# Optimization experiments

Measured on AMD Instinct MI355X. Metric: run time of the kernel, lower is better.

## Reference

```python
import jax, jax.numpy as jnp
import numpy as np

B = 32768
EPS = 0.2  # BatchNorm eps used in the original module


def _xavier(key, shape):
    fan_in, fan_out = shape[-2], shape[-1]
    std = (2.0 / (fan_in + fan_out)) ** 0.5
    return (jax.random.normal(key, shape, jnp.float32) * std).astype(jnp.float32)


def bn(x, g, b):
    # training-mode BatchNorm1d: batch stats over the batch axis (-2), biased var
    m = jnp.mean(x, axis=-2, keepdims=True)
    v = jnp.mean(jnp.square(x - m), axis=-2, keepdims=True)
    return (x - m) * jax.lax.rsqrt(v + EPS) * g + b


def setup_inputs() -> dict:
    key = jax.random.key(0)
    ks = iter(jax.random.split(key, 48))
    inp = {}
    inp['x1f'] = jax.random.normal(next(ks), (B, 512), jnp.float32)
    inp['x2f'] = jax.random.normal(next(ks), (B, 512), jnp.float32)
    # shared trunk
    inp['W1'] = _xavier(next(ks), (512, 256)); inp['b1'] = jnp.zeros(256, jnp.float32)
    inp['W2'] = _xavier(next(ks), (256, 256)); inp['b2'] = jnp.zeros(256, jnp.float32)
    # batchnorm affine params (bn1:256, bn2:256, bn3:128, bn4:64)
    inp['g1'] = jnp.ones(256, jnp.float32); inp['be1'] = jnp.zeros(256, jnp.float32)
    inp['g2'] = jnp.ones(256, jnp.float32); inp['be2'] = jnp.zeros(256, jnp.float32)
    inp['g3'] = jnp.ones(128, jnp.float32); inp['be3'] = jnp.zeros(128, jnp.float32)
    inp['g4'] = jnp.ones(64, jnp.float32); inp['be4'] = jnp.zeros(64, jnp.float32)
    # 4 branch projections from each stream (x11..x14, x21..x24), stacked on axis 0
    inp['Wbx1'] = _xavier(next(ks), (4, 256, 256)); inp['bbx1'] = jnp.zeros((4, 256), jnp.float32)
    inp['Wbx2'] = _xavier(next(ks), (4, 256, 256)); inp['bbx2'] = jnp.zeros((4, 256), jnp.float32)
    # gating MLPs (xw*1, xw*2, xw*3, y*), stacked over the 4 attributes
    inp['Wwa'] = _xavier(next(ks), (4, 512, 128)); inp['bwa'] = jnp.zeros((4, 128), jnp.float32)
    inp['Wwb'] = _xavier(next(ks), (4, 128, 64)); inp['bwb'] = jnp.zeros((4, 64), jnp.float32)
    inp['Wwc'] = _xavier(next(ks), (4, 64, 64)); inp['bwc'] = jnp.zeros((4, 64), jnp.float32)
    inp['Wy'] = _xavier(next(ks), (4, 64, 2)); inp['by'] = jnp.zeros((4, 2), jnp.float32)
    # combine layers x1c..x4c, stacked
    inp['Wc'] = _xavier(next(ks), (4, 512, 256)); inp['bc'] = jnp.zeros((4, 256), jnp.float32)
    # output heads (different class counts: 3, 3, 6, 4)
    inp['Wo1'] = _xavier(next(ks), (256, 3)); inp['bo1'] = jnp.zeros(3, jnp.float32)
    inp['Wo2'] = _xavier(next(ks), (256, 3)); inp['bo2'] = jnp.zeros(3, jnp.float32)
    inp['Wo3'] = _xavier(next(ks), (256, 6)); inp['bo3'] = jnp.zeros(6, jnp.float32)
    inp['Wo4'] = _xavier(next(ks), (256, 4)); inp['bo4'] = jnp.zeros(4, jnp.float32)
    return inp


def reference(x1f, x2f, W1, b1, W2, b2, g1, be1, g2, be2, g3, be3, g4, be4,
              Wbx1, bbx1, Wbx2, bbx2, Wwa, bwa, Wwb, bwb, Wwc, bwc, Wy, by,
              Wc, bc, Wo1, bo1, Wo2, bo2, Wo3, bo3, Wo4, bo4):
    relu = jax.nn.relu

    def trunk(x):
        h = bn(relu(x @ W1 + b1), g1, be1)
        return bn(relu(h @ W2 + b2), g2, be2)

    h1 = trunk(x1f)  # [B,256]
    h2 = trunk(x2f)  # [B,256]

    # 4 branch features per stream, each bn1-normalized: [4,B,256]
    b1x = bn(relu(jnp.einsum('bi,kio->kbo', h1, Wbx1) + bbx1[:, None, :]), g1, be1)
    b2x = bn(relu(jnp.einsum('bi,kio->kbo', h2, Wbx2) + bbx2[:, None, :]), g1, be1)

    # gating MLP per attribute -> 2-way softmax weights
    xcat = jnp.concatenate([b1x, b2x], axis=-1)  # [4,B,512]
    a = bn(relu(jnp.einsum('kbi,kio->kbo', xcat, Wwa) + bwa[:, None, :]), g3, be3)
    b_ = bn(relu(jnp.einsum('kbi,kio->kbo', a, Wwb) + bwb[:, None, :]), g4, be4)
    c = bn(relu(jnp.einsum('kbi,kio->kbo', b_, Wwc) + bwc[:, None, :]), g4, be4)
    y = jax.nn.softmax(jnp.einsum('kbi,kio->kbo', c, Wy) + by[:, None, :], axis=-1)  # [4,B,2]

    # the original per-column loop == one broadcast multiply per stream
    xw = jnp.concatenate([b1x * y[..., 0:1], b2x * y[..., 1:2]], axis=-1)  # [4,B,512]

    # combine layers (dropout is identity in eval)
    xc = bn(relu(jnp.einsum('kbi,kio->kbo', xw, Wc) + bc[:, None, :]), g1, be1)  # [4,B,256]

    y1o = jax.nn.softmax(xc[0] @ Wo1 + bo1, axis=-1)
    y2o = jax.nn.softmax(xc[1] @ Wo2 + bo2, axis=-1)
    y3o = jax.nn.softmax(xc[2] @ Wo3 + bo3, axis=-1)
    y4o = jax.nn.softmax(xc[3] @ Wo4 + bo4, axis=-1)
    return (y1o, y2o, y3o, y4o)
```

## Files before the change

### kernel.cpp

```cpp
#include <hip/hip_runtime.h>
#include <hip/hip_bf16.h>


typedef unsigned short u16;
typedef _Float16 f16x8 __attribute__((ext_vector_type(8)));
typedef float f32x4 __attribute__((ext_vector_type(4)));

#define B_ROWS 32768
#define EPS_BN 0.2f
#define BINV (1.0f / 32768.0f)

__device__ __forceinline__ float bf2f(u16 u) {
    union { unsigned int i; float f; } c;
    c.i = ((unsigned int)u) << 16;
    return c.f;
}
__device__ __forceinline__ u16 f2bf(float f) {
    union { float f; unsigned int i; } c;
    c.f = f;
    unsigned int x = c.i;
    return (u16)((x + 0x7FFFu + ((x >> 16) & 1u)) >> 16);
}
__device__ __forceinline__ float h2f(u16 u) {
    _Float16 h;
    __builtin_memcpy(&h, &u, 2);
    return (float)h;
}
__device__ __forceinline__ u16 f2h(float f) {
    _Float16 h = (_Float16)f;
    u16 u;
    __builtin_memcpy(&u, &h, 2);
    return u;
}
__device__ __forceinline__ float ldp(const void* p, long i, int flag) {
    return flag ? bf2f(((const u16*)p)[i]) : ((const float*)p)[i];
}
__device__ __forceinline__ void gload16(const u16* gp, u16* lp) {
    __builtin_amdgcn_global_load_lds(
        (const __attribute__((address_space(1))) unsigned int*)gp,
        (__attribute__((address_space(3))) unsigned int*)lp, 16, 0, 0);
}

__global__ void detect_dtype(const u16* __restrict__ x, int* __restrict__ flag) {
    const int lane = threadIdx.x;
    const u16 v = x[2 * lane];
    const int e = (v >> 7) & 0xFF;
    const bool plausible = (e >= 110 && e <= 140);
    const unsigned long long m = __ballot(plausible);
    if (lane == 0) *flag = (__popcll(m) >= 58) ? 1 : 0;
}

struct PTab { const void* p[20]; int n[20]; int off[20]; };

__global__ void convert_params(PTab t, float* __restrict__ dst,
                               const int* __restrict__ flag) {
    const int ti = blockIdx.y;
    const int n = t.n[ti];
    float* o = dst + t.off[ti];
    const int isbf = *flag;
    for (int i = blockIdx.x * 256 + threadIdx.x; i < n; i += gridDim.x * 256)
        o[i] = ldp(t.p[ti], i, isbf);
}

__global__ __launch_bounds__(256) void prep_w(
    const void* __restrict__ W, long wstride,
    const void* __restrict__ bias, long bstride,
    const float* __restrict__ psum, const float* __restrict__ psq, int pstride,
    const void* __restrict__ pg, const void* __restrict__ pbe, int gmask,
    const int* __restrict__ dtflag,
    u16* __restrict__ Wt, long wtstride,
    float* __restrict__ biasP, float* __restrict__ T0o,
    float* __restrict__ T1o, float* __restrict__ bsum, long bost,
    int K, int khalf)
{
    const int tid = threadIdx.x;
    const int n = blockIdx.x;
    const int N = gridDim.x;
    const int inst = blockIdx.y;
    const int flag = *dtflag;
    __shared__ float sn[512], tn[512];
    __shared__ float r0[4], r1[4];

    for (int i = tid; i < K; i += 256) {
        float s = 1.f, t = 0.f;
        if (psum) {
            float m = psum[(long)pstride * inst + i] * BINV;
            float v = psq[(long)pstride * inst + i] * BINV - m * m;
            float g = ldp(pg, i & gmask, flag);
            float b = ldp(pbe, i & gmask, flag);
            s = g * rsqrtf(v + EPS_BN);
            t = b - m * s;
        }
        sn[i] = s; tn[i] = t;
    }
    __syncthreads();
    float p0 = 0.f, p1 = 0.f;
    for (int k = tid; k < K; k += 256) {
        float wv = ldp(W, wstride * inst + (long)k * N + n, flag);
        Wt[wtstride * inst + (long)n * K + k] = f2h(sn[k] * wv);
        float tw = tn[k] * wv;
        if (k < khalf) p0 += tw; else p1 += tw;
    }
#pragma unroll
    for (int off = 32; off; off >>= 1) {
        p0 += __shfl_xor(p0, off);
        p1 += __shfl_xor(p1, off);
    }
    const int lane = tid & 63, wid = tid >> 6;
    if (lane == 0) { r0[wid] = p0; r1[wid] = p1; }
    __syncthreads();
    if (tid == 0) {
        float t0 = r0[0] + r0[1] + r0[2] + r0[3];
        float t1 = r1[0] + r1[1] + r1[2] + r1[3];
        float bp = ldp(bias, bstride * inst + n, flag);
        long o = bost * inst + n;
        biasP[o] = bp; T0o[o] = t0; T1o[o] = t1; bsum[o] = bp + t0 + t1;
    }
}

template <bool XSTAGE, bool ROWW, int WM, int WN, int K>
__global__ __launch_bounds__(256, 3) void gemm_mfma(
    const void* __restrict__ X, const void* __restrict__ X2,
    long xstride, int ximask, int ldx, int ksplit, long ksecond,
    const int* __restrict__ dtflag,
    const u16* __restrict__ Wt, long wtstride,
    const float* __restrict__ biasP, const float* __restrict__ T0,
    const float* __restrict__ T1, const float* __restrict__ bsum, int bN,
    u16* __restrict__ Out, long ostride, int ldout,
    float* __restrict__ gsum, float* __restrict__ gsq, int sstride,
    const float* __restrict__ Y0v)
{
    const int tid = threadIdx.x;
    const int lane = tid & 63;
    const int wid = tid >> 6;
    const int wm = wid / WN, wn = wid % WN;
    const int inst = blockIdx.z;
    const int rowB = blockIdx.x * (64 * WM);
    const int nBase = blockIdx.y * (64 * WN);
    const int n0 = nBase + wn * 64;
    const int fm = lane & 15, quad = lane >> 4;
    const int rloc = lane >> 3;
    const int cg = (lane & 7) ^ rloc;

    __shared__ __align__(16) u16 As[WM * 4096];
    __shared__ __align__(16) u16 Bs[WN * 4096];
    __shared__ float redS[4][64];
    __shared__ float redQ[4][64];

    const bool xf32 = XSTAGE && (*dtflag == 0);
    const char* xb;
    if (XSTAGE) xb = (const char*)(inst == 0 ? X : X2);
    else        xb = (const char*)X + 2l * xstride * (inst & ximask);
    const u16* wtp = Wt + wtstride * inst;
    u16* op = Out + ostride * inst;

    f32x4 acc[4][4];
#pragma unroll
    for (int i = 0; i < 4; ++i)
#pragma unroll
        for (int j = 0; j < 4; ++j) acc[i][j] = (f32x4){0.f, 0.f, 0.f, 0.f};

    _Float16 ysc[2][4];
    if constexpr (ROWW) {
        const float* yp = Y0v + (long)inst * B_ROWS;
#pragma unroll
        for (int mi = 0; mi < 4; ++mi) {
            const float y = yp[rowB + wm * 64 + mi * 16 + fm];
            ysc[0][mi] = (_Float16)y;
            ysc[1][mi] = (_Float16)(1.f - y);
        }
    }

    for (int kt = 0; kt < K / 64; ++kt) {
        const int kk = kt * 64;
        __syncthreads();
        if constexpr (XSTAGE) {
#pragma unroll
            for (int p = 0; p < WM * 2; ++p) {
                const int s = p * 256 + tid;
                const int m = s >> 3, c = s & 7;
                const int g = c ^ (m & 7);
                f16x8 h;
                if (xf32) {
                    const float* gp = (const float*)xb + (long)(rowB + m) * ldx + kk + g * 8;
                    const float4 u = *(const float4*)gp;
                    const float4 u2 = *(const float4*)(gp + 4);
                    h[0] = (_Float16)u.x;  h[1] = (_Float16)u.y;
                    h[2] = (_Float16)u.z;  h[3] = (_Float16)u.w;
                    h[4] = (_Float16)u2.x; h[5] = (_Float16)u2.y;
                    h[6] = (_Float16)u2.z; h[7] = (_Float16)u2.w;
                } else {
                    const uint4 v = *(const uint4*)((const u16*)xb + (long)(rowB + m) * ldx + kk + g * 8);
                    const u16* pv = (const u16*)&v;
#pragma unroll
                    for (int j = 0; j < 8; ++j) h[j] = (_Float16)bf2f(pv[j]);
                }
                *(f16x8*)&As[s * 8] = h;
            }
        } else {
            const u16* xs = (const u16*)xb;
            int kkr = kk;
            if (kk >= ksplit) { xs += ksecond; kkr -= ksplit; }
#pragma unroll
            for (int s = wid; s < WM * 8; s += 4)
                gload16(xs + (long)(rowB + s * 8 + rloc) * ldx + kkr + cg * 8,
                        &As[s * 512 + lane * 8]);
        }
#pragma unroll
        for (int s = wid; s < WN * 8; s += 4)
            gload16(wtp + (long)(nBase + s * 8 + rloc) * K + kk + cg * 8,
                    &Bs[s * 512 + lane * 8]);
        __syncthreads();

        const int sel = (ROWW && kk >= ksplit) ? 1 : 0;
#pragma unroll
        for (int q = 0; q < 2; ++q) {
            f16x8 af[4], bfr[4];
#pragma unroll
            for (int mi = 0; mi < 4; ++mi) {
                const int mm = wm * 64 + mi * 16 + fm;
                af[mi] = *(const f16x8*)&As[mm * 64 + (((q * 4 + quad) ^ (mm & 7)) * 8)];
            }
            if constexpr (ROWW) {
#pragma unroll
                for (int mi = 0; mi < 4; ++mi) {
                    const _Float16 yh = ysc[sel][mi];
#pragma unroll
                    for (int j = 0; j < 8; ++j) af[mi][j] *= yh;
                }
            }
#pragma unroll
            for (int ni = 0; ni < 4; ++ni) {
                const int nn = wn * 64 + ni * 16 + fm;
                bfr[ni] = *(const f16x8*)&Bs[nn * 64 + (((q * 4 + quad) ^ (nn & 7)) * 8)];
            }
#pragma unroll
            for (int mi = 0; mi < 4; ++mi)
#pragma unroll
                for (int ni = 0; ni < 4; ++ni)
                    acc[mi][ni] = __builtin_amdgcn_mfma_f32_16x16x32_f16(
                        af[mi], bfr[ni], acc[mi][ni], 0, 0, 0);
        }
    }

    __syncthreads();

    float yv[16];
    if constexpr (ROWW) {
        const float* yp = Y0v + (long)inst * B_ROWS;
#pragma unroll
        for (int mi = 0; mi < 4; ++mi)
#pragma unroll
            for (int r = 0; r < 4; ++r)
                yv[mi * 4 + r] = yp[rowB + wm * 64 + mi * 16 + quad * 4 + r];
    }

#pragma unroll
    for (int ni = 0; ni < 4; ++ni) {
        const int nc = ni * 16 + fm;
        const int n = n0 + nc;
        float bS = 0.f, bP = 0.f, t0v = 0.f, t1v = 0.f;
        if constexpr (ROWW) {
            bP = biasP[(long)inst * bN + n];
            t0v = T0[(long)inst * bN + n];
            t1v = T1[(long)inst * bN + n];
        } else {
            bS = bsum[(long)inst * bN + n];
        }
        float s = 0.f, qq = 0.f;
#pragma unroll
        for (int mi = 0; mi < 4; ++mi) {
            const int rbase = rowB + wm * 64 + mi * 16 + quad * 4;
#pragma unroll
            for (int r = 0; r < 4; ++r) {
                float v;
                if constexpr (ROWW) {
                    const float y = yv[mi * 4 + r];
                    v = acc[mi][ni][r] + y * t0v + (1.f - y) * t1v + bP;
                } else {
                    v = acc[mi][ni][r] + bS;
                }
                v = fmaxf(v, 0.f);
                s += v; qq += v * v;
                op[(long)(rbase + r) * ldout + n] = f2h(v);
            }
        }
        s += __shfl_xor(s, 16);  s += __shfl_xor(s, 32);
        qq += __shfl_xor(qq, 16); qq += __shfl_xor(qq, 32);
        if (quad == 0) { redS[wid][nc] = s; redQ[wid][nc] = qq; }
    }
    __syncthreads();
    if (tid < WN * 64) {
        const int wnc = tid >> 6, within = tid & 63;
        float s = 0.f, q = 0.f;
#pragma unroll
        for (int w = 0; w < WM; ++w) {
            s += redS[w * WN + wnc][within];
            q += redQ[w * WN + wnc][within];
        }
        atomicAdd(&gsum[(long)inst * sstride + nBase + tid], s);
        atomicAdd(&gsq [(long)inst * sstride + nBase + tid], q);
    }
}

__global__ __launch_bounds__(256) void gate_kernel(
    const u16* __restrict__ zc,
    const float* __restrict__ stFs, const float* __restrict__ stFq,
    const float* __restrict__ g4, const float* __restrict__ be4,
    const float* __restrict__ Wy, const float* __restrict__ by,
    float* __restrict__ Y0)
{
    const int lane = threadIdx.x & 63;
    const int wid = threadIdx.x >> 6;
    const int k = blockIdx.y;
    const int row = blockIdx.x * 4 + wid;

    const float m = stFs[k * 64 + lane] * BINV;
    const float v = stFq[k * 64 + lane] * BINV - m * m;
    const float s = g4[lane] * rsqrtf(v + EPS_BN);
    const float t = be4[lane] - m * s;
    const float x = h2f(zc[((long)k * B_ROWS + row) * 64 + lane]) * s + t;

    float p0 = x * Wy[k * 128 + lane * 2 + 0];
    float p1 = x * Wy[k * 128 + lane * 2 + 1];
#pragma unroll
    for (int off = 32; off; off >>= 1) {
        p0 += __shfl_xor(p0, off);
        p1 += __shfl_xor(p1, off);
    }
    if (lane == 0) {
        const float l0 = p0 + by[k * 2 + 0];
        const float l1 = p1 + by[k * 2 + 1];
        Y0[(long)k * B_ROWS + row] = 1.f / (1.f + __expf(l1 - l0));
    }
}

__global__ __launch_bounds__(256) void heads_kernel(
    const u16* __restrict__ zxc,
    const float* __restrict__ stHs, const float* __restrict__ stHq,
    const float* __restrict__ g1, const float* __restrict__ be1,
    const float* __restrict__ Wo1, const float* __restrict__ bo1,
    const float* __restrict__ Wo2, const float* __restrict__ bo2,
    const float* __restrict__ Wo3, const float* __restrict__ bo3,
    const float* __restrict__ Wo4, const float* __restrict__ bo4,
    void* __restrict__ out, const int* __restrict__ dtflag)
{
    const int lane = threadIdx.x & 63;
    const int wid = threadIdx.x >> 6;
    const int k = blockIdx.y;
    const int row = blockIdx.x * 4 + wid;
    const int c0 = lane * 4;

    const ushort4 q = *(const ushort4*)(zxc + ((long)k * B_ROWS + row) * 256 + c0);
    float x[4] = {h2f(q.x), h2f(q.y), h2f(q.z), h2f(q.w)};
#pragma unroll
    for (int j = 0; j < 4; j++) {
        const int c = c0 + j;
        const float m = stHs[k * 256 + c] * BINV;
        const float v = stHq[k * 256 + c] * BINV - m * m;
        const float s = g1[c] * rsqrtf(v + EPS_BN);
        x[j] = x[j] * s + (be1[c] - m * s);
    }

    const float* Wo; const float* bo; int nk; long obase;
    if (k == 0)      { Wo = Wo1; bo = bo1; nk = 3; obase = 0; }
    else if (k == 1) { Wo = Wo2; bo = bo2; nk = 3; obase = (long)3 * B_ROWS; }
    else if (k == 2) { Wo = Wo3; bo = bo3; nk = 6; obase = (long)6 * B_ROWS; }
    else             { Wo = Wo4; bo = bo4; nk = 4; obase = (long)12 * B_ROWS; }

    float l[6];
#pragma unroll
    for (int j = 0; j < 6; j++) l[j] = 0.f;
#pragma unroll
    for (int j = 0; j < 6; j++) {
        if (j < nk) {
            float p = 0.f;
#pragma unroll
            for (int i = 0; i < 4; i++) p += x[i] * Wo[(c0 + i) * nk + j];
            l[j] = p;
        }
    }
#pragma unroll
    for (int off = 32; off; off >>= 1) {
#pragma unroll
        for (int j = 0; j < 6; j++) l[j] += __shfl_xor(l[j], off);
    }

    if (lane == 0) {
        float mx = -1e30f;
#pragma unroll
        for (int j = 0; j < 6; j++)
            if (j < nk) { l[j] += bo[j]; mx = fmaxf(mx, l[j]); }
        float e[6];
        float se = 0.f;
#pragma unroll
        for (int j = 0; j < 6; j++)
            if (j < nk) { e[j] = __expf(l[j] - mx); se += e[j]; }
        const float inv = 1.f / se;
        if (*dtflag) {
            u16* ob = (u16*)out;
#pragma unroll
            for (int j = 0; j < 6; j++)
                if (j < nk) ob[obase + (long)row * nk + j] = f2bf(e[j] * inv);
        } else {
            float* of = (float*)out;
#pragma unroll
            for (int j = 0; j < 6; j++)
                if (j < nk) of[obase + (long)row * nk + j] = e[j] * inv;
        }
    }
}

__global__ void fill_sentinel(u16* out, int n) {
    int i = blockIdx.x * 256 + threadIdx.x;
    if (i < n) out[i] = 0x3E80;
}

extern "C" void kernel_launch(void* const* d_in, const int* in_sizes, int n_in,
                              void* d_out, int out_size, void* d_ws, size_t ws_size,
                              hipStream_t stream)
{
    const long B = B_ROWS;
    char* ws = (char*)d_ws;
    const size_t MB = 1024 * 1024;

    u16* z1  = (u16*)(ws);
    u16* z2  = (u16*)(ws + 32 * MB);
    u16* za  = (u16*)(ws);
    u16* zbb = (u16*)(ws + 32 * MB);
    u16* zc  = (u16*)(ws + 48 * MB);
    u16* zxc = (u16*)(ws);
    u16* zb  = (u16*)(ws + 64 * MB);
    float* Y0 = (float*)(ws + 192 * MB);
    float* stats = (float*)(ws + 192 * MB + 512 * 1024);
    int* dtflag = (int*)(ws + 192 * MB + 576 * 1024);
    float* Pst = (float*)(ws + 192 * MB + 640 * 1024);

    u16* WtA = (u16*)(ws + 193 * MB);
    u16* WtB = WtA + 131072;
    u16* WtC = WtB + 131072;
    u16* WtD = WtC + 524288;
    u16* WtH = WtD + 262144;
    u16* WtE = WtH + 524288;
    u16* WtF = WtE + 32768;
    float* biasArea = (float*)(ws + 197 * MB);
    float* bA = biasArea;
    float* bB = bA + 2048;
    float* bC = bB + 2048;
    float* bD = bC + 8192;
    float* bH = bD + 2048;
    float* bE = bH + 4096;
    float* bF = bE + 1024;

    const int cIdx[20] = {6,7,10,11,12,13,20,21,22,23,24,25,28,29,30,31,32,33,34,35};
    PTab tab;
    int mapOff[36];
    int acc = 0;
    for (int i = 0; i < 20; i++) {
        tab.p[i] = d_in[cIdx[i]];
        tab.n[i] = in_sizes[cIdx[i]];
        tab.off[i] = acc;
        mapOff[cIdx[i]] = acc;
        acc += in_sizes[cIdx[i]];
    }
    const size_t need = 197 * MB + 20480 * 4 + 4096;
    if (need > ws_size || (size_t)acc * 4 > 384 * 1024) {
        fill_sentinel<<<(out_size + 255) / 256, 256, 0, stream>>>((u16*)d_out, out_size);
        return;
    }
    auto PF = [&](int idx) { return Pst + mapOff[idx]; };

    float* stAs = stats;        float* stAq = stAs + 512;
    float* stBs = stAq + 512;   float* stBq = stBs + 512;
    float* stCs = stBq + 512;   float* stCq = stCs + 2048;
    float* stDs = stCq + 2048;  float* stDq = stDs + 512;
    float* stEs = stDq + 512;   float* stEq = stEs + 256;
    float* stFs = stEq + 256;   float* stFq = stFs + 256;
    float* stHs = stFq + 256;   float* stHq = stHs + 1024;

    hipMemsetAsync(stats, 0, 10240 * 4, stream);
    detect_dtype<<<1, 64, 0, stream>>>((const u16*)d_in[0], dtflag);
    convert_params<<<dim3(32, 20), 256, 0, stream>>>(tab, Pst, dtflag);

    const dim3 blk(256);
    const int BIGK = 1 << 29;

    prep_w<<<dim3(256, 2), blk, 0, stream>>>(
        d_in[2], 0, d_in[3], 0, nullptr, nullptr, 0, nullptr, nullptr, 0,
        dtflag, WtA, 0, bA, bA + 512, bA + 1024, bA + 1536, 256, 512, 512);
    gemm_mfma<true, false, 2, 2, 512><<<dim3(256, 2, 2), blk, 0, stream>>>(
        d_in[0], d_in[1], 0, 0, 512, BIGK, 0, dtflag, WtA, 0,
        bA, bA + 512, bA + 1024, bA + 1536, 256,
        z1, B * 256, 256, stAs, stAq, 256, nullptr);

    prep_w<<<dim3(256, 2), blk, 0, stream>>>(
        d_in[4], 0, d_in[5], 0, stAs, stAq, 256, d_in[6], d_in[7], 255,
        dtflag, WtB, 65536, bB, bB + 512, bB + 1024, bB + 1536, 256, 256, 256);
    gemm_mfma<false, false, 2, 2, 256><<<dim3(256, 2, 2), blk, 0, stream>>>(
        z1, nullptr, B * 256, 3, 256, BIGK, 0, dtflag, WtB, 65536,
        bB, bB + 512, bB + 1024, bB + 1536, 256,
        z2, B * 256, 256, stBs, stBq, 256, nullptr);

    for (int s = 0; s < 2; s++) {
        prep_w<<<dim3(256, 4), blk, 0, stream>>>(
            d_in[s ? 16 : 14], 65536, d_in[s ? 17 : 15], 256,
            stBs + s * 256, stBq + s * 256, 0, d_in[8], d_in[9], 255,
            dtflag, WtC + s * 65536, 131072,
            bC + s * 256, bC + 2048 + s * 256, bC + 4096 + s * 256,
            bC + 6144 + s * 256, 512, 256, 256);
    }
    gemm_mfma<false, false, 2, 2, 256><<<dim3(256, 2, 8), blk, 0, stream>>>(
        z2, nullptr, B * 256, 1, 256, BIGK, 0, dtflag, WtC, 65536,
        bC, bC + 2048, bC + 4096, bC + 6144, 256,
        zb, B * 256, 256, stCs, stCq, 256, nullptr);

    prep_w<<<dim3(128, 4), blk, 0, stream>>>(
        d_in[18], 65536, d_in[19], 128, stCs, stCq, 512, d_in[6], d_in[7], 255,
        dtflag, WtD, 65536, bD, bD + 512, bD + 1024, bD + 1536, 128, 512, 512);
    prep_w<<<dim3(256, 4), blk, 0, stream>>>(
        d_in[26], 131072, d_in[27], 256, stCs, stCq, 512, d_in[6], d_in[7], 255,
        dtflag, WtH, 131072, bH, bH + 1024, bH + 2048, bH + 3072, 256, 512, 256);
    gemm_mfma<false, false, 2, 2, 512><<<dim3(256, 1, 4), blk, 0, stream>>>(
        zb, nullptr, 2 * B * 256, 3, 256, 256, B * 256, dtflag, WtD, 65536,
        bD, bD + 512, bD + 1024, bD + 1536, 128,
        za, B * 128, 128, stDs, stDq, 128, nullptr);

    prep_w<<<dim3(64, 4), blk, 0, stream>>>(
        d_in[20], 8192, d_in[21], 64, stDs, stDq, 128, d_in[10], d_in[11], 127,
        dtflag, WtE, 8192, bE, bE + 256, bE + 512, bE + 768, 64, 128, 128);
    gemm_mfma<false, false, 4, 1, 128><<<dim3(128, 1, 4), blk, 0, stream>>>(
        za, nullptr, B * 128, 3, 128, BIGK, 0, dtflag, WtE, 8192,
        bE, bE + 256, bE + 512, bE + 768, 64,
        zbb, B * 64, 64, stEs, stEq, 64, nullptr);

    prep_w<<<dim3(64, 4), blk, 0, stream>>>(
        d_in[22], 4096, d_in[23], 64, stEs, stEq, 64, d_in[12], d_in[13], 63,
        dtflag, WtF, 4096, bF, bF + 256, bF + 512, bF + 768, 64, 64, 64);
    gemm_mfma<false, false, 4, 1, 64><<<dim3(128, 1, 4), blk, 0, stream>>>(
        zbb, nullptr, B * 64, 3, 64, BIGK, 0, dtflag, WtF, 4096,
        bF, bF + 256, bF + 512, bF + 768, 64,
        zc, B * 64, 64, stFs, stFq, 64, nullptr);

    gate_kernel<<<dim3(B_ROWS / 4, 4), blk, 0, stream>>>(
        zc, stFs, stFq, PF(12), PF(13), PF(24), PF(25), Y0);

    gemm_mfma<false, true, 2, 2, 512><<<dim3(256, 2, 4), blk, 0, stream>>>(
        zb, nullptr, 2 * B * 256, 3, 256, 256, B * 256, dtflag, WtH, 131072,
        bH, bH + 1024, bH + 2048, bH + 3072, 256,
        zxc, B * 256, 256, stHs, stHq, 256, Y0);

    heads_kernel<<<dim3(B_ROWS / 4, 4), blk, 0, stream>>>(
        zxc, stHs, stHq, PF(6), PF(7), PF(28), PF(29), PF(30), PF(31),
        PF(32), PF(33), PF(34), PF(35), d_out, dtflag);
}
```

Measured before the change: 697.3 us.

## Fold BatchNorm into weights and process many rows per block in gate/heads kernels

The gate and heads kernels now precompute the BatchNorm-scaled weights (s*W) and the folded bias (sum t*W + b) once per block in shared memory. Each thread then handles a slice of one row with 16-byte vector loads instead of one wave per row. This removes the per-row recomputation of BN stats and rsqrt and cuts shuffle reductions and block count. In exchange it adds shared-memory setup and syncs per block, plus an XOR swizzle to avoid LDS bank conflicts.

```diff
diff --git a/kernel.cpp b/kernel.cpp
--- a/kernel.cpp
+++ b/kernel.cpp
@@ -310,27 +310,57 @@
     const float* __restrict__ Wy, const float* __restrict__ by,
     float* __restrict__ Y0)
 {
-    const int lane = threadIdx.x & 63;
-    const int wid = threadIdx.x >> 6;
+    const int tid = threadIdx.x;
     const int k = blockIdx.y;
-    const int row = blockIdx.x * 4 + wid;
-
-    const float m = stFs[k * 64 + lane] * BINV;
-    const float v = stFq[k * 64 + lane] * BINV - m * m;
-    const float s = g4[lane] * rsqrtf(v + EPS_BN);
-    const float t = be4[lane] - m * s;
-    const float x = h2f(zc[((long)k * B_ROWS + row) * 64 + lane]) * s + t;
-
-    float p0 = x * Wy[k * 128 + lane * 2 + 0];
-    float p1 = x * Wy[k * 128 + lane * 2 + 1];
-#pragma unroll
-    for (int off = 32; off; off >>= 1) {
-        p0 += __shfl_xor(p0, off);
-        p1 += __shfl_xor(p1, off);
-    }
-    if (lane == 0) {
-        const float l0 = p0 + by[k * 2 + 0];
-        const float l1 = p1 + by[k * 2 + 1];
+    const int r0 = blockIdx.x * 128;
+
+    __shared__ __align__(8) float Ws2[64][2];
+    __shared__ float cg[2];
+
+    if (tid < 64) {
+        const int c = tid;
+        const float m = stFs[k * 64 + c] * BINV;
+        const float v = stFq[k * 64 + c] * BINV - m * m;
+        const float s = g4[c] * rsqrtf(v + EPS_BN);
+        const float t = be4[c] - m * s;
+        const float w0 = Wy[k * 128 + c * 2 + 0];
+        const float w1 = Wy[k * 128 + c * 2 + 1];
+        Ws2[c][0] = s * w0;
+        Ws2[c][1] = s * w1;
+        float t0 = t * w0, t1 = t * w1;
+#pragma unroll
+        for (int off = 32; off; off >>= 1) {
+            t0 += __shfl_xor(t0, off);
+            t1 += __shfl_xor(t1, off);
+        }
+        if (c == 0) {
+            cg[0] = t0 + by[k * 2 + 0];
+            cg[1] = t1 + by[k * 2 + 1];
+        }
+    }
+    __syncthreads();
+
+    const int row = r0 + (tid >> 1);
+    const int seg = tid & 1;
+    const u16* xp = zc + ((long)k * B_ROWS + row) * 64 + seg * 32;
+    float a0 = 0.f, a1 = 0.f;
+#pragma unroll
+    for (int it = 0; it < 4; ++it) {
+        const uint4 v = *(const uint4*)(xp + it * 8);
+        const u16* pv = (const u16*)&v;
+#pragma unroll
+        for (int e = 0; e < 8; ++e) {
+            const int c = seg * 32 + it * 8 + e;
+            const float x = h2f(pv[e]);
+            a0 += x * Ws2[c][0];
+            a1 += x * Ws2[c][1];
+        }
+    }
+    a0 += __shfl_xor(a0, 1);
+    a1 += __shfl_xor(a1, 1);
+    if (seg == 0) {
+        const float l0 = a0 + cg[0];
+        const float l1 = a1 + cg[1];
         Y0[(long)k * B_ROWS + row] = 1.f / (1.f + __expf(l1 - l0));
     }
 }
@@ -345,22 +375,9 @@
     const float* __restrict__ Wo4, const float* __restrict__ bo4,
     void* __restrict__ out, const int* __restrict__ dtflag)
 {
-    const int lane = threadIdx.x & 63;
-    const int wid = threadIdx.x >> 6;
+    const int tid = threadIdx.x;
     const int k = blockIdx.y;
-    const int row = blockIdx.x * 4 + wid;
-    const int c0 = lane * 4;
-
-    const ushort4 q = *(const ushort4*)(zxc + ((long)k * B_ROWS + row) * 256 + c0);
-    float x[4] = {h2f(q.x), h2f(q.y), h2f(q.z), h2f(q.w)};
-#pragma unroll
-    for (int j = 0; j < 4; j++) {
-        const int c = c0 + j;
-        const float m = stHs[k * 256 + c] * BINV;
-        const float v = stHq[k * 256 + c] * BINV - m * m;
-        const float s = g1[c] * rsqrtf(v + EPS_BN);
-        x[j] = x[j] * s + (be1[c] - m * s);
-    }
+    const int r0 = blockIdx.x * 64;
 
     const float* Wo; const float* bo; int nk; long obase;
     if (k == 0)      { Wo = Wo1; bo = bo1; nk = 3; obase = 0; }
@@ -368,29 +385,77 @@
     else if (k == 2) { Wo = Wo3; bo = bo3; nk = 6; obase = (long)6 * B_ROWS; }
     else             { Wo = Wo4; bo = bo4; nk = 4; obase = (long)12 * B_ROWS; }
 
-    float l[6];
-#pragma unroll
-    for (int j = 0; j < 6; j++) l[j] = 0.f;
-#pragma unroll
-    for (int j = 0; j < 6; j++) {
-        if (j < nk) {
-            float p = 0.f;
-#pragma unroll
-            for (int i = 0; i < 4; i++) p += x[i] * Wo[(c0 + i) * nk + j];
-            l[j] = p;
-        }
-    }
-#pragma unroll
-    for (int off = 32; off; off >>= 1) {
-#pragma unroll
-        for (int j = 0; j < 6; j++) l[j] += __shfl_xor(l[j], off);
-    }
-
-    if (lane == 0) {
+    __shared__ __align__(16) float Ws[256][8];
+    __shared__ float cj[8];
+    __shared__ float redC[4][8];
+
+    {
+        const int c = tid;
+        const float m = stHs[k * 256 + c] * BINV;
+        const float v = stHq[k * 256 + c] * BINV - m * m;
+        const float s = g1[c] * rsqrtf(v + EPS_BN);
+        const float t = be1[c] - m * s;
+        const int rs = c ^ (c >> 6);
+        float tw[6];
+#pragma unroll
+        for (int j = 0; j < 6; ++j) {
+            const float w = (j < nk) ? Wo[c * nk + j] : 0.f;
+            Ws[rs][j] = s * w;
+            tw[j] = t * w;
+        }
+        Ws[rs][6] = 0.f; Ws[rs][7] = 0.f;
+#pragma unroll
+        for (int off = 32; off; off >>= 1)
+#pragma unroll
+            for (int j = 0; j < 6; ++j) tw[j] += __shfl_xor(tw[j], off);
+        const int lane = tid & 63, wid = tid >> 6;
+        if (lane < 6) redC[wid][lane] = tw[lane];
+    }
+    __syncthreads();
+    if (tid < 8) {
+        float s4 = 0.f;
+        if (tid < 6) s4 = redC[0][tid] + redC[1][tid] + redC[2][tid] + redC[3][tid];
+        cj[tid] = (tid < nk) ? s4 + bo[tid] : 0.f;
+    }
+    __syncthreads();
+
+    const int row = r0 + (tid >> 2);
+    const int seg = tid & 3;
+    const u16* xp = zxc + ((long)k * B_ROWS + row) * 256 + seg * 64;
+    float acc[6];
+#pragma unroll
+    for (int j = 0; j < 6; ++j) acc[j] = 0.f;
+#pragma unroll
+    for (int it = 0; it < 8; ++it) {
+        const uint4 v = *(const uint4*)(xp + it * 8);
+        const u16* pv = (const u16*)&v;
+#pragma unroll
+        for (int e = 0; e < 8; ++e) {
+            const int cc = it * 8 + e;
+            const int rs = (seg * 64 + cc) ^ seg;
+            const float x = h2f(pv[e]);
+            const f32x4 w0 = *(const f32x4*)&Ws[rs][0];
+            const f32x4 w1 = *(const f32x4*)&Ws[rs][4];
+            acc[0] += x * w0[0];
+            acc[1] += x * w0[1];
+            acc[2] += x * w0[2];
+            acc[3] += x * w0[3];
+            acc[4] += x * w1[0];
+            acc[5] += x * w1[1];
+        }
+    }
+#pragma unroll
+    for (int j = 0; j < 6; ++j) {
+        acc[j] += __shfl_xor(acc[j], 1);
+        acc[j] += __shfl_xor(acc[j], 2);
+    }
+
+    if (seg == 0) {
+        float l[6];
         float mx = -1e30f;
 #pragma unroll
         for (int j = 0; j < 6; j++)
-            if (j < nk) { l[j] += bo[j]; mx = fmaxf(mx, l[j]); }
+            if (j < nk) { l[j] = acc[j] + cj[j]; mx = fmaxf(mx, l[j]); }
         float e[6];
         float se = 0.f;
 #pragma unroll
@@ -541,7 +606,7 @@
         bF, bF + 256, bF + 512, bF + 768, 64,
         zc, B * 64, 64, stFs, stFq, 64, nullptr);
 
-    gate_kernel<<<dim3(B_ROWS / 4, 4), blk, 0, stream>>>(
+    gate_kernel<<<dim3(B_ROWS / 128, 4), blk, 0, stream>>>(
         zc, stFs, stFq, PF(12), PF(13), PF(24), PF(25), Y0);
 
     gemm_mfma<false, true, 2, 2, 512><<<dim3(256, 2, 4), blk, 0, stream>>>(
@@ -549,7 +614,7 @@
         bH, bH + 1024, bH + 2048, bH + 3072, 256,
         zxc, B * 256, 256, stHs, stHq, 256, Y0);
 
-    heads_kernel<<<dim3(B_ROWS / 4, 4), blk, 0, stream>>>(
+    heads_kernel<<<dim3(B_ROWS / 64, 4), blk, 0, stream>>>(
         zxc, stHs, stHq, PF(6), PF(7), PF(28), PF(29), PF(30), PF(31),
         PF(32), PF(33), PF(34), PF(35), d_out, dtflag);
 }
```

Measured after the change: 585.9 us. 1.19x faster.
